# Kernel optimization log

Measured on AMD Instinct MI355X. Metric: run time of the kernel, lower is better.

Reference implementation:

```python
import jax, jax.numpy as jnp
import numpy as np

N_NODES = 100000
N_EDGES = 1600000
IN_F = 128
HID = 16
NEG_SLOPE = 0.2


def setup_inputs() -> dict:
    key = jax.random.key(0)
    ks = jax.random.split(key, 12)
    x = jax.random.normal(ks[0], (N_NODES, IN_F), dtype=jnp.float32)
    edge_index = jax.random.randint(ks[1], (2, N_EDGES), 0, N_NODES, dtype=jnp.int32)
    s1 = 1.0 / np.sqrt(IN_F)
    s2 = 1.0 / np.sqrt(2 * HID)
    # layer 1: heads=2, out=16, concat -> 32
    W1 = jax.random.normal(ks[2], (IN_F, 2 * HID), dtype=jnp.float32) * s1
    a_src1 = jax.random.normal(ks[3], (2, HID), dtype=jnp.float32) * s2
    a_dst1 = jax.random.normal(ks[4], (2, HID), dtype=jnp.float32) * s2
    b1 = jnp.zeros((2 * HID,), dtype=jnp.float32)
    # layer 2: heads=1, out=1
    W2 = jax.random.normal(ks[5], (2 * HID, 1), dtype=jnp.float32) * s2
    a_src2 = jax.random.normal(ks[6], (1, 1), dtype=jnp.float32)
    a_dst2 = jax.random.normal(ks[7], (1, 1), dtype=jnp.float32)
    b2 = jnp.zeros((1,), dtype=jnp.float32)
    return {"x": x, "edge_index": edge_index, "W1": W1, "a_src1": a_src1,
            "a_dst1": a_dst1, "b1": b1, "W2": W2, "a_src2": a_src2,
            "a_dst2": a_dst2, "b2": b2}


def gat_conv(x, src, dst, W, a_src, a_dst, bias, heads, out_ch, concat):
    # PyG GATConv: linear proj, per-edge leaky-relu score, segment softmax over
    # incoming edges (dst), scatter-add aggregation. Self loops already in src/dst.
    n = x.shape[0]
    h = (x @ W).reshape(n, heads, out_ch)                      # [N,H,C]
    alpha_s = (h * a_src[None]).sum(-1)                        # [N,H]
    alpha_d = (h * a_dst[None]).sum(-1)                        # [N,H]
    e = jax.nn.leaky_relu(alpha_s[src] + alpha_d[dst], NEG_SLOPE)  # [E,H]
    m = jax.lax.stop_gradient(jax.ops.segment_max(e, dst, num_segments=n))
    ex = jnp.exp(e - m[dst])
    denom = jax.ops.segment_sum(ex, dst, num_segments=n)       # [N,H]
    alpha = ex / (denom[dst] + 1e-16)                          # [E,H]
    out = jax.ops.segment_sum(alpha[..., None] * h[src], dst, num_segments=n)  # [N,H,C]
    out = out.reshape(n, heads * out_ch) if concat else out.mean(axis=1)
    return out + bias


def reference(x, edge_index, W1, a_src1, a_dst1, b1, W2, a_src2, a_dst2, b2):
    n = x.shape[0]
    loop = jnp.arange(n, dtype=edge_index.dtype)
    src = jnp.concatenate([edge_index[0], loop])
    dst = jnp.concatenate([edge_index[1], loop])
    h = jax.nn.elu(gat_conv(x, src, dst, W1, a_src1, a_dst1, b1, 2, HID, True))
    out = gat_conv(h, src, dst, W2, a_src2, a_dst2, b2, 1, 1, False)
    return out
```

## Files before the change

kernel.cpp:

```cpp
#include <hip/hip_runtime.h>
#include <math.h>

#define IN_F 128
#define C1 32
#define NEG 0.2f
#define BSZ 64
#define CAPB 1312
#define EPB 2048
#define TPW 2
#define HISTN 1664

typedef _Float16 h16;
typedef _Float16 h16x2 __attribute__((ext_vector_type(2)));
typedef _Float16 h16x4 __attribute__((ext_vector_type(4)));
typedef _Float16 h16x8 __attribute__((ext_vector_type(8)));
typedef float f32x4 __attribute__((ext_vector_type(4)));

__device__ __forceinline__ float leaky(float x) { return x >= 0.f ? x : NEG * x; }

__global__ __launch_bounds__(256)
void k_fat(const float* __restrict__ x, const float* __restrict__ W1,
           const float* __restrict__ a_s, const float* __restrict__ a_d,
           h16* __restrict__ h1h, float* __restrict__ as1,
           float* __restrict__ ad1, int N,
           const int* __restrict__ ei, int E, int ET, int nbk,
           int* __restrict__ bcnt, int* __restrict__ ebuf, int nproj) {
    __shared__ int smem[2 * HISTN + 4096];
    int t = threadIdx.x;
    if ((int)blockIdx.x < nproj) {
        int wid = t >> 6, lane = t & 63;
        int q = lane >> 4, r = lane & 15;
        h16x8 Bf[2][4];
        #pragma unroll
        for (int ct = 0; ct < 2; ++ct)
            #pragma unroll
            for (int kc = 0; kc < 4; ++kc)
                #pragma unroll
                for (int j = 0; j < 8; ++j)
                    Bf[ct][kc][j] = (h16)W1[(kc * 32 + q * 8 + j) * C1 + ct * 16 + r];
        float a_s0 = a_s[r], a_s1v = a_s[16 + r];
        float a_d0 = a_d[r], a_d1v = a_d[16 + r];
        #pragma unroll
        for (int tt = 0; tt < TPW; ++tt) {
            int tile = (blockIdx.x * 4 + wid) * TPW + tt;
            int m0 = tile << 4;
            if (m0 >= N) break;
            int row = m0 + r; if (row >= N) row = N - 1;
            const float* xr = x + (size_t)row * IN_F + q * 8;
            f32x4 acc0 = {0.f, 0.f, 0.f, 0.f};
            f32x4 acc1 = {0.f, 0.f, 0.f, 0.f};
            #pragma unroll
            for (int kc = 0; kc < 4; ++kc) {
                float4 xa = *(const float4*)(xr + kc * 32);
                float4 xb = *(const float4*)(xr + kc * 32 + 4);
                h16x8 A;
                A[0] = (h16)xa.x; A[1] = (h16)xa.y; A[2] = (h16)xa.z; A[3] = (h16)xa.w;
                A[4] = (h16)xb.x; A[5] = (h16)xb.y; A[6] = (h16)xb.z; A[7] = (h16)xb.w;
                acc0 = __builtin_amdgcn_mfma_f32_16x16x32_f16(A, Bf[0][kc], acc0, 0, 0, 0);
                acc1 = __builtin_amdgcn_mfma_f32_16x16x32_f16(A, Bf[1][kc], acc1, 0, 0, 0);
            }
            #pragma unroll
            for (int reg = 0; reg < 4; ++reg) {
                int node = m0 + q * 4 + reg;
                bool vld = node < N;
                float h0 = acc0[reg], h1 = acc1[reg];
                if (vld) {
                    h1h[(size_t)node * C1 + r]      = (h16)h0;
                    h1h[(size_t)node * C1 + 16 + r] = (h16)h1;
                }
                float s0 = h0 * a_s0, s1 = h1 * a_s1v;
                float d0 = h0 * a_d0, d1 = h1 * a_d1v;
                s0 += __shfl_xor(s0, 1); s0 += __shfl_xor(s0, 2); s0 += __shfl_xor(s0, 4); s0 += __shfl_xor(s0, 8);
                s1 += __shfl_xor(s1, 1); s1 += __shfl_xor(s1, 2); s1 += __shfl_xor(s1, 4); s1 += __shfl_xor(s1, 8);
                d0 += __shfl_xor(d0, 1); d0 += __shfl_xor(d0, 2); d0 += __shfl_xor(d0, 4); d0 += __shfl_xor(d0, 8);
                d1 += __shfl_xor(d1, 1); d1 += __shfl_xor(d1, 2); d1 += __shfl_xor(d1, 4); d1 += __shfl_xor(d1, 8);
                if (vld && r == 0) {
                    *(float2*)&as1[node * 2] = make_float2(s0, s1);
                    *(float2*)&ad1[node * 2] = make_float2(d0, d1);
                }
            }
        }
    } else {
        int* hist = smem;
        int* lcur = smem + HISTN;
        int2* ecache = (int2*)(smem + 2 * HISTN);
        int bid = blockIdx.x - nproj;
        for (int b = t; b < nbk; b += 256) hist[b] = 0;
        __syncthreads();
        int i0 = bid * EPB, i1 = min(ET, i0 + EPB);
        for (int i = i0 + t; i < i1; i += 256) {
            int s, d;
            if (i < E) { s = ei[i]; d = ei[E + i]; } else { s = d = i - E; }
            ecache[i - i0] = make_int2(s, d);
            atomicAdd(&hist[d >> 6], 1);
        }
        __syncthreads();
        for (int b = t; b < nbk; b += 256) {
            int h = hist[b];
            int base = h ? atomicAdd(&bcnt[b], h) : 0;
            lcur[b] = b * CAPB + base;
        }
        __syncthreads();
        for (int i = i0 + t; i < i1; i += 256) {
            int2 e = ecache[i - i0];
            int bkt = e.y >> 6;
            int pos = atomicAdd(&lcur[bkt], 1);
            if (pos < (bkt + 1) * CAPB)
                ebuf[pos] = (e.x << 6) | (e.y & 63);
        }
    }
}

__global__ __launch_bounds__(256)
void k_bagg(const int* __restrict__ bcnt, const int* __restrict__ ebuf,
            int N, int nbk, int ET,
            const float* __restrict__ as1, const float* __restrict__ ad1,
            const float* __restrict__ b1, const float* __restrict__ W2,
            const h16* __restrict__ h1h, int* __restrict__ off,
            int* __restrict__ csr1, float* __restrict__ p2) {
    __shared__ int2 elist[CAPB];
    __shared__ int deg[BSZ], sst[BSZ], cur[BSZ];
    __shared__ float adl[BSZ * 2];
    __shared__ float b1s[C1], w2s[C1];
    __shared__ int red[4];
    int b = blockIdx.x, t = threadIdx.x;
    int n0 = b * BSZ;
    int cnt = min(bcnt[b], CAPB);
    int ebase = b * CAPB;
    int part = 0;
    for (int k = t; k < b; k += 256) part += min(bcnt[k], CAPB);
    part += __shfl_xor(part, 1);  part += __shfl_xor(part, 2);
    part += __shfl_xor(part, 4);  part += __shfl_xor(part, 8);
    part += __shfl_xor(part, 16); part += __shfl_xor(part, 32);
    if ((t & 63) == 0) red[t >> 6] = part;
    if (t < BSZ) {
        deg[t] = 0;
        int n = n0 + t;
        float2 v = (n < N) ? ((const float2*)ad1)[n] : make_float2(0.f, 0.f);
        adl[t * 2] = v.x; adl[t * 2 + 1] = v.y;
    }
    if (t >= 64 && t < 64 + C1) { b1s[t - 64] = b1[t - 64]; w2s[t - 64] = W2[t - 64]; }
    if (b == nbk - 1 && t == 0) off[N] = ET;
    __syncthreads();
    int fbase = red[0] + red[1] + red[2] + red[3];
    for (int i = t; i < cnt; i += 256)
        atomicAdd(&deg[ebuf[ebase + i] & 63], 1);
    __syncthreads();
    if (t < 64) {
        int orig = deg[t], v = orig;
        #pragma unroll
        for (int o = 1; o < 64; o <<= 1) {
            int u = __shfl_up(v, o);
            if (t >= o) v += u;
        }
        deg[t] = v;
        int e = v - orig;
        sst[t] = e; cur[t] = e;
        if (n0 + t < N) off[n0 + t] = fbase + e;
    }
    __syncthreads();
    for (int i = t; i < cnt; i += 256) {
        int e = ebuf[ebase + i];
        int dl = e & 63, s = e >> 6;
        float2 asv = ((const float2*)as1)[s];
        float w0 = __expf(leaky(asv.x + adl[dl * 2 + 0]));
        float w1 = __expf(leaky(asv.y + adl[dl * 2 + 1]));
        h16x2 wp = { (h16)w0, (h16)w1 };
        int p = atomicAdd(&cur[dl], 1);
        int2 rec; rec.x = s; rec.y = *(int*)&wp;
        elist[p] = rec;
        csr1[fbase + p] = s;
    }
    __syncthreads();
    int l = t & 3, slot = t >> 2, c0 = l * 8, head = l >> 1;
    int node = n0 + slot;
    if (node >= N) return;
    int j0 = sst[slot], j1 = deg[slot];
    float den = 0.f;
    float acc[8] = {0.f, 0.f, 0.f, 0.f, 0.f, 0.f, 0.f, 0.f};
    for (int j = j0; j < j1; j += 8) {
        #pragma unroll
        for (int k = 0; k < 8; ++k) {
            int jj = j + k;
            bool valid = jj < j1;
            jj = valid ? jj : j0;
            int2 e = elist[jj];
            int s = e.x;
            h16x2 wv = *(h16x2*)&e.y;
            float w = valid ? (float)(head ? wv.y : wv.x) : 0.f;
            h16x8 hv = *(const h16x8*)(h1h + ((size_t)s << 5) + c0);
            den += w;
            #pragma unroll
            for (int i2 = 0; i2 < 8; ++i2)
                acc[i2] = fmaf(w, (float)hv[i2], acc[i2]);
        }
    }
    float inv = 1.f / (den + 1e-16f);
    float val = 0.f;
    #pragma unroll
    for (int i2 = 0; i2 < 8; ++i2) {
        float o = acc[i2] * inv + b1s[c0 + i2];
        o = o > 0.f ? o : expm1f(o);
        val = fmaf(o, w2s[c0 + i2], val);
    }
    val += __shfl_xor(val, 1); val += __shfl_xor(val, 2);
    if (l == 0) p2[node] = val;
}

__global__ __launch_bounds__(256)
void k_l2(const int* __restrict__ off, const int* __restrict__ csr1,
          const float* __restrict__ p2, const float* __restrict__ as2,
          const float* __restrict__ ad2, const float* __restrict__ b2,
          float* __restrict__ out, int N) {
    int tid = blockIdx.x * 256 + threadIdx.x;
    int g = tid >> 3, l = tid & 7;
    if (g >= N) return;
    float A = as2[0];
    float Bc = ad2[0] * p2[g];
    float den = 0.f, num = 0.f;
    int j0 = off[g], j1 = off[g + 1];
    for (int j = j0 + l; j < j1; j += 8) {
        float ps = p2[csr1[j]];
        float w = __expf(leaky(fmaf(ps, A, Bc)));
        den += w;
        num = fmaf(w, ps, num);
    }
    den += __shfl_xor(den, 1); den += __shfl_xor(den, 2); den += __shfl_xor(den, 4);
    num += __shfl_xor(num, 1); num += __shfl_xor(num, 2); num += __shfl_xor(num, 4);
    if (l == 0) out[g] = num / (den + 1e-16f) + b2[0];
}

extern "C" void kernel_launch(void* const* d_in, const int* in_sizes, int n_in,
                              void* d_out, int out_size, void* d_ws, size_t ws_size,
                              hipStream_t stream) {
    const float* x    = (const float*)d_in[0];
    const int*   ei   = (const int*)d_in[1];
    const float* W1   = (const float*)d_in[2];
    const float* a_s1 = (const float*)d_in[3];
    const float* a_d1 = (const float*)d_in[4];
    const float* b1   = (const float*)d_in[5];
    const float* W2   = (const float*)d_in[6];
    const float* a_s2 = (const float*)d_in[7];
    const float* a_d2 = (const float*)d_in[8];
    const float* b2   = (const float*)d_in[9];
    float* out = (float*)d_out;

    const int N  = in_sizes[0] / IN_F;
    const int E  = in_sizes[1] / 2;
    const int ET = E + N;
    const int nbk = (N + BSZ - 1) / BSZ;

    float* w   = (float*)d_ws;
    float* as1 = w; w += (size_t)2 * N;
    float* ad1 = w; w += (size_t)2 * N;
    float* p2  = w; w += (size_t)N;
    h16* h1h   = (h16*)w;
    w += (size_t)16 * N;
    int* iw     = (int*)w;
    int* bcnt   = iw; iw += 2048;
    int* off    = iw; iw += (N + 1);
    int* csr1   = iw; iw += ET;
    int* ebuf   = iw; iw += (size_t)nbk * CAPB;

    const int B = 256;
    const int ntile = (N + 15) / 16;
    const int nproj = (ntile + 4 * TPW - 1) / (4 * TPW);
    const int nblkA = (ET + EPB - 1) / EPB;

    hipMemsetAsync(bcnt, 0, 2048 * sizeof(int), stream);
    k_fat <<<nproj + nblkA, B, 0, stream>>>(x, W1, a_s1, a_d1, h1h, as1, ad1, N,
                                            ei, E, ET, nbk, bcnt, ebuf, nproj);
    k_bagg<<<nbk, B, 0, stream>>>(bcnt, ebuf, N, nbk, ET, as1, ad1, b1, W2,
                                  h1h, off, csr1, p2);
    k_l2  <<<(N * 8 + B - 1) / B, B, 0, stream>>>(off, csr1, p2, a_s2, a_d2, b2, out, N);
}
```

Baseline: 182.7 us.

## Drop CSR construction; run layer 2 directly over bucketed edge buffer

Layer 2 now reads the per-bucket edge buffer and accumulates softmax numerator and denominator with shared-memory float atomics for each 64-node bucket. This lets k_bagg skip the prefix sum over bucket counts and the writes of the CSR offsets and source arrays. The edge cache in k_fat is also packed into an int plus a ushort per edge, and the histogram array is reused as the cursor array, which reduces shared memory. The costs are shared-atomic contention on high-degree nodes and a nondeterministic float summation order.

```diff
diff --git a/kernel.cpp b/kernel.cpp
--- a/kernel.cpp
+++ b/kernel.cpp
@@ -25,7 +25,7 @@
            float* __restrict__ ad1, int N,
            const int* __restrict__ ei, int E, int ET, int nbk,
            int* __restrict__ bcnt, int* __restrict__ ebuf, int nproj) {
-    __shared__ int smem[2 * HISTN + 4096];
+    __shared__ int smem[HISTN + EPB + EPB / 2];
     int t = threadIdx.x;
     if ((int)blockIdx.x < nproj) {
         int wid = t >> 6, lane = t & 63;
@@ -82,8 +82,8 @@
         }
     } else {
         int* hist = smem;
-        int* lcur = smem + HISTN;
-        int2* ecache = (int2*)(smem + 2 * HISTN);
+        int* er   = smem + HISTN;
+        unsigned short* eb = (unsigned short*)(smem + HISTN + EPB);
         int bid = blockIdx.x - nproj;
         for (int b = t; b < nbk; b += 256) hist[b] = 0;
         __syncthreads();
@@ -91,48 +91,40 @@
         for (int i = i0 + t; i < i1; i += 256) {
             int s, d;
             if (i < E) { s = ei[i]; d = ei[E + i]; } else { s = d = i - E; }
-            ecache[i - i0] = make_int2(s, d);
+            er[i - i0] = (s << 6) | (d & 63);
+            eb[i - i0] = (unsigned short)(d >> 6);
             atomicAdd(&hist[d >> 6], 1);
         }
         __syncthreads();
         for (int b = t; b < nbk; b += 256) {
             int h = hist[b];
             int base = h ? atomicAdd(&bcnt[b], h) : 0;
-            lcur[b] = b * CAPB + base;
+            hist[b] = b * CAPB + base;
         }
         __syncthreads();
         for (int i = i0 + t; i < i1; i += 256) {
-            int2 e = ecache[i - i0];
-            int bkt = e.y >> 6;
-            int pos = atomicAdd(&lcur[bkt], 1);
+            int bkt = eb[i - i0];
+            int pos = atomicAdd(&hist[bkt], 1);
             if (pos < (bkt + 1) * CAPB)
-                ebuf[pos] = (e.x << 6) | (e.y & 63);
+                ebuf[pos] = er[i - i0];
         }
     }
 }
 
 __global__ __launch_bounds__(256)
 void k_bagg(const int* __restrict__ bcnt, const int* __restrict__ ebuf,
-            int N, int nbk, int ET,
+            int N, int nbk,
             const float* __restrict__ as1, const float* __restrict__ ad1,
             const float* __restrict__ b1, const float* __restrict__ W2,
-            const h16* __restrict__ h1h, int* __restrict__ off,
-            int* __restrict__ csr1, float* __restrict__ p2) {
+            const h16* __restrict__ h1h, float* __restrict__ p2) {
     __shared__ int2 elist[CAPB];
     __shared__ int deg[BSZ], sst[BSZ], cur[BSZ];
     __shared__ float adl[BSZ * 2];
     __shared__ float b1s[C1], w2s[C1];
-    __shared__ int red[4];
     int b = blockIdx.x, t = threadIdx.x;
     int n0 = b * BSZ;
     int cnt = min(bcnt[b], CAPB);
     int ebase = b * CAPB;
-    int part = 0;
-    for (int k = t; k < b; k += 256) part += min(bcnt[k], CAPB);
-    part += __shfl_xor(part, 1);  part += __shfl_xor(part, 2);
-    part += __shfl_xor(part, 4);  part += __shfl_xor(part, 8);
-    part += __shfl_xor(part, 16); part += __shfl_xor(part, 32);
-    if ((t & 63) == 0) red[t >> 6] = part;
     if (t < BSZ) {
         deg[t] = 0;
         int n = n0 + t;
@@ -140,9 +132,7 @@
         adl[t * 2] = v.x; adl[t * 2 + 1] = v.y;
     }
     if (t >= 64 && t < 64 + C1) { b1s[t - 64] = b1[t - 64]; w2s[t - 64] = W2[t - 64]; }
-    if (b == nbk - 1 && t == 0) off[N] = ET;
-    __syncthreads();
-    int fbase = red[0] + red[1] + red[2] + red[3];
+    __syncthreads();
     for (int i = t; i < cnt; i += 256)
         atomicAdd(&deg[ebuf[ebase + i] & 63], 1);
     __syncthreads();
@@ -156,7 +146,6 @@
         deg[t] = v;
         int e = v - orig;
         sst[t] = e; cur[t] = e;
-        if (n0 + t < N) off[n0 + t] = fbase + e;
     }
     __syncthreads();
     for (int i = t; i < cnt; i += 256) {
@@ -169,7 +158,6 @@
         int p = atomicAdd(&cur[dl], 1);
         int2 rec; rec.x = s; rec.y = *(int*)&wp;
         elist[p] = rec;
-        csr1[fbase + p] = s;
     }
     __syncthreads();
     int l = t & 3, slot = t >> 2, c0 = l * 8, head = l >> 1;
@@ -208,26 +196,33 @@
 }
 
 __global__ __launch_bounds__(256)
-void k_l2(const int* __restrict__ off, const int* __restrict__ csr1,
+void k_l2(const int* __restrict__ bcnt, const int* __restrict__ ebuf,
           const float* __restrict__ p2, const float* __restrict__ as2,
           const float* __restrict__ ad2, const float* __restrict__ b2,
           float* __restrict__ out, int N) {
-    int tid = blockIdx.x * 256 + threadIdx.x;
-    int g = tid >> 3, l = tid & 7;
-    if (g >= N) return;
+    __shared__ float den[BSZ], num[BSZ], pdl[BSZ];
+    int b = blockIdx.x, t = threadIdx.x;
+    int n0 = b * BSZ;
+    if (t < BSZ) {
+        den[t] = 0.f; num[t] = 0.f;
+        int n = n0 + t;
+        pdl[t] = (n < N) ? ad2[0] * p2[n] : 0.f;
+    }
+    __syncthreads();
     float A = as2[0];
-    float Bc = ad2[0] * p2[g];
-    float den = 0.f, num = 0.f;
-    int j0 = off[g], j1 = off[g + 1];
-    for (int j = j0 + l; j < j1; j += 8) {
-        float ps = p2[csr1[j]];
-        float w = __expf(leaky(fmaf(ps, A, Bc)));
-        den += w;
-        num = fmaf(w, ps, num);
-    }
-    den += __shfl_xor(den, 1); den += __shfl_xor(den, 2); den += __shfl_xor(den, 4);
-    num += __shfl_xor(num, 1); num += __shfl_xor(num, 2); num += __shfl_xor(num, 4);
-    if (l == 0) out[g] = num / (den + 1e-16f) + b2[0];
+    int cnt = min(bcnt[b], CAPB);
+    int ebase = b * CAPB;
+    for (int i = t; i < cnt; i += 256) {
+        int e = ebuf[ebase + i];
+        int dl = e & 63, s = e >> 6;
+        float ps = p2[s];
+        float w = __expf(leaky(fmaf(ps, A, pdl[dl])));
+        atomicAdd(&den[dl], w);
+        atomicAdd(&num[dl], w * ps);
+    }
+    __syncthreads();
+    if (t < BSZ && n0 + t < N)
+        out[n0 + t] = num[t] / (den[t] + 1e-16f) + b2[0];
 }
 
 extern "C" void kernel_launch(void* const* d_in, const int* in_sizes, int n_in,
@@ -258,8 +253,6 @@
     w += (size_t)16 * N;
     int* iw     = (int*)w;
     int* bcnt   = iw; iw += 2048;
-    int* off    = iw; iw += (N + 1);
-    int* csr1   = iw; iw += ET;
     int* ebuf   = iw; iw += (size_t)nbk * CAPB;
 
     const int B = 256;
@@ -270,7 +263,6 @@
     hipMemsetAsync(bcnt, 0, 2048 * sizeof(int), stream);
     k_fat <<<nproj + nblkA, B, 0, stream>>>(x, W1, a_s1, a_d1, h1h, as1, ad1, N,
                                             ei, E, ET, nbk, bcnt, ebuf, nproj);
-    k_bagg<<<nbk, B, 0, stream>>>(bcnt, ebuf, N, nbk, ET, as1, ad1, b1, W2,
-                                  h1h, off, csr1, p2);
-    k_l2  <<<(N * 8 + B - 1) / B, B, 0, stream>>>(off, csr1, p2, a_s2, a_d2, b2, out, N);
-}
+    k_bagg<<<nbk, B, 0, stream>>>(bcnt, ebuf, N, nbk, as1, ad1, b1, W2, h1h, p2);
+    k_l2  <<<nbk, B, 0, stream>>>(bcnt, ebuf, p2, a_s2, a_d2, b2, out, N);
+}
```

New measurement: 186.9 us. 2.3% more time.
